# Kernel optimization log

Hardware: AMD Instinct MI355X
Metric: run time of the kernel (lower is better)

The kernel has to match this reference:

```python
import jax, jax.numpy as jnp
import numpy as np

D_MODEL = 1024
D_HEAD = 64
B, S = 4, 2048


def setup_inputs() -> dict:
    key = jax.random.key(0)
    k1, k2, k3, k4 = jax.random.split(key, 4)
    residual_stream = jax.random.normal(k1, (B, S, D_MODEL), dtype=jnp.float32)
    # torch.nn.Linear weights are [out_features, in_features]
    Wq = jax.random.normal(k2, (D_HEAD, D_MODEL), dtype=jnp.float32) * 0.02
    Wk = jax.random.normal(k3, (D_HEAD, D_MODEL), dtype=jnp.float32) * 0.02
    Wv = jax.random.normal(k4, (D_HEAD, D_MODEL), dtype=jnp.float32) * 0.02
    return {"residual_stream": residual_stream, "Wq": Wq, "Wk": Wk, "Wv": Wv}


def reference(residual_stream, Wq, Wk, Wv):
    # Linear projections (no bias): y = x @ W.T
    q = jnp.einsum('bsd,hd->bsh', residual_stream, Wq)  # [B,S,d_head]
    k = jnp.einsum('bsd,hd->bsh', residual_stream, Wk)
    v = jnp.einsum('bsd,hd->bsh', residual_stream, Wv)
    # NOTE: module scales by 1/sqrt(d_model), not 1/sqrt(d_head)
    scale = 1.0 / jnp.sqrt(jnp.float32(D_MODEL))
    scores = jnp.einsum('bqh,bkh->bqk', q, k) * scale  # [B,S,S]
    # causal mask: lower-triangular allowed
    s = residual_stream.shape[1]
    causal = jnp.tril(jnp.ones((s, s), dtype=bool))
    scores = jnp.where(causal[None, :, :], scores, -jnp.inf)
    attn = jax.nn.softmax(scores, axis=-1)
    # dropout_chance=0.0 (eval/deterministic) -> identity
    return jnp.einsum('bqk,bkh->bqh', attn, v)  # [B,S,d_head]
```

## Files before the change

### kernel.cpp

```cpp
#include <hip/hip_runtime.h>
#include <hip/hip_bf16.h>

#define NB 4
#define SEQ 2048
#define DM 1024
#define DH 64

typedef __attribute__((ext_vector_type(8))) short bf16x8;
typedef __attribute__((ext_vector_type(4))) float f32x4;
typedef __attribute__((ext_vector_type(4))) short short4v;

__device__ inline short f2bf(float f) {
  union { float f; unsigned u; } x; x.f = f;
  unsigned r = x.u + 0x7FFFu + ((x.u >> 16) & 1u);
  return (short)(r >> 16);
}

__global__ __launch_bounds__(256) void wconv_kernel(
    const float* __restrict__ Wq, const float* __restrict__ Wk,
    const float* __restrict__ Wv, short* __restrict__ wbf)
{
  const int tid = blockIdx.x * 256 + threadIdx.x;
  const int base = tid * 8;
  const int row = base >> 10;
  const int col = base & 1023;
  const float* src = (row < 64) ? Wq : (row < 128) ? Wk : Wv;
  src += (size_t)(row & 63) * DM + col;
  f32x4 f0 = ((const f32x4*)src)[0];
  f32x4 f1 = ((const f32x4*)src)[1];
  bf16x8 h = { f2bf(f0[0]), f2bf(f0[1]), f2bf(f0[2]), f2bf(f0[3]),
               f2bf(f1[0]), f2bf(f1[1]), f2bf(f1[2]), f2bf(f1[3]) };
  *(bf16x8*)(wbf + (size_t)row * DM + col) = h;
}

__global__ __launch_bounds__(512) void proj_kernel(
    const float* __restrict__ X, const short* __restrict__ wbf,
    short* __restrict__ qout, short* __restrict__ kout,
    short* __restrict__ vtout)
{
  __shared__ short x_lds[2][32][80];
  __shared__ short w_lds[2][192][80];

  const int t = threadIdx.x;
  const int l = t & 63;
  const int w = t >> 6;
  const int m0 = blockIdx.x * 32;

  f32x4 acc[3];
#pragma unroll
  for (int i = 0; i < 3; i++) acc[i] = (f32x4){0.f, 0.f, 0.f, 0.f};

  const int xr = t >> 4;
  const int xc = (t & 15) * 4;
  const int wr = t >> 3;
  const int wc = (t & 7) * 8;

  const float* xsrc  = X   + (size_t)(m0 + xr) * DM + xc;
  const short* wsrc0 = wbf + (size_t)(wr)       * DM + wc;
  const short* wsrc1 = wbf + (size_t)(64 + wr)  * DM + wc;
  const short* wsrc2 = wbf + (size_t)(128 + wr) * DM + wc;

  {
    f32x4 f = *(const f32x4*)xsrc;
    short4v h = { f2bf(f[0]), f2bf(f[1]), f2bf(f[2]), f2bf(f[3]) };
    *(short4v*)&x_lds[0][xr][xc] = h;
    *(bf16x8*)&w_lds[0][wr][wc]       = *(const bf16x8*)wsrc0;
    *(bf16x8*)&w_lds[0][64 + wr][wc]  = *(const bf16x8*)wsrc1;
    *(bf16x8*)&w_lds[0][128 + wr][wc] = *(const bf16x8*)wsrc2;
  }
  f32x4 xA = *(const f32x4*)(xsrc + 64);
  bf16x8 wA0 = *(const bf16x8*)(wsrc0 + 64);
  bf16x8 wA1 = *(const bf16x8*)(wsrc1 + 64);
  bf16x8 wA2 = *(const bf16x8*)(wsrc2 + 64);
  f32x4 xB;
  bf16x8 wB0, wB1, wB2;
  __syncthreads();

#pragma unroll
  for (int it = 0; it < 16; it++) {
    const int buf = it & 1;
    const int k2 = (it + 2) * 64;

    if ((it & 1) == 0) {
      if (it + 2 < 16) {
        xB  = *(const f32x4*)(xsrc + k2);
        wB0 = *(const bf16x8*)(wsrc0 + k2);
        wB1 = *(const bf16x8*)(wsrc1 + k2);
        wB2 = *(const bf16x8*)(wsrc2 + k2);
      }
    } else {
      if (it + 2 < 16) {
        xA  = *(const f32x4*)(xsrc + k2);
        wA0 = *(const bf16x8*)(wsrc0 + k2);
        wA1 = *(const bf16x8*)(wsrc1 + k2);
        wA2 = *(const bf16x8*)(wsrc2 + k2);
      }
    }

    const short* xp = &x_lds[buf][(w & 1) * 16 + (l & 15)][(l >> 4) << 3];
    bf16x8 a0 = *(const bf16x8*)xp;
    bf16x8 a1 = *(const bf16x8*)(xp + 32);
#pragma unroll
    for (int nf = 0; nf < 3; nf++) {
      const int cf = (w >> 1) * 3 + nf;
      const short* wp = &w_lds[buf][cf * 16 + (l & 15)][(l >> 4) << 3];
      bf16x8 b0 = *(const bf16x8*)wp;
      bf16x8 b1 = *(const bf16x8*)(wp + 32);
      acc[nf] = __builtin_amdgcn_mfma_f32_16x16x32_bf16(a0, b0, acc[nf], 0, 0, 0);
      acc[nf] = __builtin_amdgcn_mfma_f32_16x16x32_bf16(a1, b1, acc[nf], 0, 0, 0);
    }

    if (it < 15) {
      if ((it & 1) == 0) {
        short4v h = { f2bf(xA[0]), f2bf(xA[1]), f2bf(xA[2]), f2bf(xA[3]) };
        *(short4v*)&x_lds[buf ^ 1][xr][xc] = h;
        *(bf16x8*)&w_lds[buf ^ 1][wr][wc]       = wA0;
        *(bf16x8*)&w_lds[buf ^ 1][64 + wr][wc]  = wA1;
        *(bf16x8*)&w_lds[buf ^ 1][128 + wr][wc] = wA2;
      } else {
        short4v h = { f2bf(xB[0]), f2bf(xB[1]), f2bf(xB[2]), f2bf(xB[3]) };
        *(short4v*)&x_lds[buf ^ 1][xr][xc] = h;
        *(bf16x8*)&w_lds[buf ^ 1][wr][wc]       = wB0;
        *(bf16x8*)&w_lds[buf ^ 1][64 + wr][wc]  = wB1;
        *(bf16x8*)&w_lds[buf ^ 1][128 + wr][wc] = wB2;
      }
    }
    __syncthreads();
  }

  const int rowb = m0 + (w & 1) * 16 + ((l >> 4) << 2);
#pragma unroll
  for (int nf = 0; nf < 3; nf++) {
    const int c = ((w >> 1) * 3 + nf) * 16 + (l & 15);
#pragma unroll
    for (int j = 0; j < 4; j++) {
      const int row = rowb + j;
      const float v = acc[nf][j];
      if (c < 64) {
        qout[row * DH + c] = f2bf(v * 0.03125f);
      } else if (c < 128) {
        kout[row * DH + (c - 64)] = f2bf(v);
      } else {
        const int b = row >> 11, s = row & (SEQ - 1);
        vtout[b * (DH * SEQ) + (c - 128) * SEQ + s] = f2bf(v);
      }
    }
  }
}

__global__ __launch_bounds__(256) void flash_kernel(
    const short* __restrict__ qin, const short* __restrict__ kin,
    const short* __restrict__ vtin, float* __restrict__ po,
    float* __restrict__ pm, float* __restrict__ pl,
    const int nck, const int cht)
{
  __shared__ short k_lds[2][64][72];
  __shared__ short vt_lds[2][64][72];
  __shared__ short p_lds[4][16][72];

  const int qt = blockIdx.x;
  const int ck = blockIdx.y;
  const int t0 = ck * cht;
  if (t0 > qt) return;
  const int b = blockIdx.z;

  const int t = threadIdx.x;
  const int l = t & 63;
  const int w = t >> 6;
  const int q0 = qt * 64;
  const int tend = min(t0 + cht, qt + 1);

  const short* qb = qin  + (size_t)b * SEQ * DH;
  const short* kb = kin  + (size_t)b * SEQ * DH;
  const short* vb = vtin + (size_t)b * DH * SEQ;

  const short* qr = qb + (size_t)(q0 + w * 16 + (l & 15)) * DH + ((l >> 4) << 3);
  const bf16x8 qf0 = *(const bf16x8*)qr;
  const bf16x8 qf1 = *(const bf16x8*)(qr + 32);

  f32x4 o[4];
#pragma unroll
  for (int i = 0; i < 4; i++) o[i] = (f32x4){0.f, 0.f, 0.f, 0.f};
  float m_run[4] = {-1e30f, -1e30f, -1e30f, -1e30f};
  float l_run[4] = {0.f, 0.f, 0.f, 0.f};

  const int sr = t >> 3;
  const int sc = (t & 7) * 8;

  {
    const int j0 = t0 * 64;
#pragma unroll
    for (int i = 0; i < 2; i++) {
      const int r = sr + i * 32;
      *(bf16x8*)&k_lds[0][r][sc]  = *(const bf16x8*)(kb + (size_t)(j0 + r) * DH + sc);
      *(bf16x8*)&vt_lds[0][r][sc] = *(const bf16x8*)(vb + (size_t)r * SEQ + j0 + sc);
    }
  }
  __syncthreads();

  for (int tt = t0; tt < tend; tt++) {
    const int bi = (tt - t0) & 1;
    const int j0 = tt * 64;
    const bool pf = (tt + 1 < tend);

    bf16x8 kpf0, kpf1, vpf0, vpf1;
    if (pf) {
      const int j1 = j0 + 64;
      kpf0 = *(const bf16x8*)(kb + (size_t)(j1 + sr) * DH + sc);
      kpf1 = *(const bf16x8*)(kb + (size_t)(j1 + sr + 32) * DH + sc);
      vpf0 = *(const bf16x8*)(vb + (size_t)sr * SEQ + j1 + sc);
      vpf1 = *(const bf16x8*)(vb + (size_t)(sr + 32) * SEQ + j1 + sc);
    }

    f32x4 s[4];
#pragma unroll
    for (int nf = 0; nf < 4; nf++) {
      const short* kr = &k_lds[bi][nf * 16 + (l & 15)][(l >> 4) << 3];
      bf16x8 b0 = *(const bf16x8*)kr;
      bf16x8 b1 = *(const bf16x8*)(kr + 32);
      f32x4 a = (f32x4){0.f, 0.f, 0.f, 0.f};
      a = __builtin_amdgcn_mfma_f32_16x16x32_bf16(qf0, b0, a, 0, 0, 0);
      a = __builtin_amdgcn_mfma_f32_16x16x32_bf16(qf1, b1, a, 0, 0, 0);
      s[nf] = a;
    }

    {
      const int growb = q0 + w * 16 + ((l >> 4) << 2);
#pragma unroll
      for (int nf = 0; nf < 4; nf++) {
        const int gcol = j0 + nf * 16 + (l & 15);
#pragma unroll
        for (int j = 0; j < 4; j++)
          if (gcol > growb + j) s[nf][j] = -1e30f;
      }
    }

    float alpha[4];
#pragma unroll
    for (int j = 0; j < 4; j++) {
      float tm = fmaxf(fmaxf(s[0][j], s[1][j]), fmaxf(s[2][j], s[3][j]));
      tm = fmaxf(tm, __shfl_xor(tm, 1));
      tm = fmaxf(tm, __shfl_xor(tm, 2));
      tm = fmaxf(tm, __shfl_xor(tm, 4));
      tm = fmaxf(tm, __shfl_xor(tm, 8));
      const float mn = fmaxf(m_run[j], tm);
      alpha[j] = exp2f((m_run[j] - mn) * 1.44269504f);
      m_run[j] = mn;
      float rs = 0.f;
#pragma unroll
      for (int nf = 0; nf < 4; nf++) {
        const float p = exp2f((s[nf][j] - mn) * 1.44269504f);
        s[nf][j] = p;
        rs += p;
      }
      rs += __shfl_xor(rs, 1);
      rs += __shfl_xor(rs, 2);
      rs += __shfl_xor(rs, 4);
      rs += __shfl_xor(rs, 8);
      l_run[j] = l_run[j] * alpha[j] + rs;
    }
#pragma unroll
    for (int df = 0; df < 4; df++)
#pragma unroll
      for (int j = 0; j < 4; j++) o[df][j] *= alpha[j];

#pragma unroll
    for (int nf = 0; nf < 4; nf++)
#pragma unroll
      for (int j = 0; j < 4; j++)
        p_lds[w][((l >> 4) << 2) + j][nf * 16 + (l & 15)] = f2bf(s[nf][j]);

    asm volatile("s_waitcnt lgkmcnt(0)" ::: "memory");
    __builtin_amdgcn_sched_barrier(0);

#pragma unroll
    for (int ks = 0; ks < 2; ks++) {
      const short* pr = &p_lds[w][l & 15][ks * 32 + ((l >> 4) << 3)];
      const bf16x8 pa = *(const bf16x8*)pr;
#pragma unroll
      for (int df = 0; df < 4; df++) {
        const short* vr = &vt_lds[bi][df * 16 + (l & 15)][ks * 32 + ((l >> 4) << 3)];
        const bf16x8 vf = *(const bf16x8*)vr;
        o[df] = __builtin_amdgcn_mfma_f32_16x16x32_bf16(pa, vf, o[df], 0, 0, 0);
      }
    }

    if (pf) {
      *(bf16x8*)&k_lds[bi ^ 1][sr][sc]       = kpf0;
      *(bf16x8*)&k_lds[bi ^ 1][sr + 32][sc]  = kpf1;
      *(bf16x8*)&vt_lds[bi ^ 1][sr][sc]      = vpf0;
      *(bf16x8*)&vt_lds[bi ^ 1][sr + 32][sc] = vpf1;
    }
    __syncthreads();
  }

  const int rowb = q0 + w * 16 + ((l >> 4) << 2);
#pragma unroll
  for (int j = 0; j < 4; j++) {
    const size_t rowg = (size_t)b * SEQ + rowb + j;
#pragma unroll
    for (int df = 0; df < 4; df++)
      po[(rowg * nck + ck) * DH + df * 16 + (l & 15)] = o[df][j];
    if ((l & 15) == 0) {
      pm[rowg * nck + ck] = m_run[j];
      pl[rowg * nck + ck] = l_run[j];
    }
  }
}

__global__ __launch_bounds__(256) void merge_kernel(
    const float* __restrict__ po, const float* __restrict__ pm,
    const float* __restrict__ pl, float* __restrict__ out,
    const int nck, const int ckshift)
{
  const int gid = blockIdx.x * 256 + threadIdx.x;
  const int r = gid >> 6;
  const int d = gid & 63;
  const int s = r & (SEQ - 1);
  const int C = (s >> ckshift) + 1;

  float m = -1e30f;
  for (int c = 0; c < C; c++) m = fmaxf(m, pm[r * nck + c]);
  float den = 0.f, num = 0.f;
  for (int c = 0; c < C; c++) {
    const float wgt = exp2f((pm[r * nck + c] - m) * 1.44269504f);
    den += pl[r * nck + c] * wgt;
    num += po[(size_t)(r * nck + c) * DH + d] * wgt;
  }
  out[gid] = num / den;
}

extern "C" void kernel_launch(void* const* d_in, const int* in_sizes, int n_in,
                              void* d_out, int out_size, void* d_ws, size_t ws_size,
                              hipStream_t stream) {
  const float* X  = (const float*)d_in[0];
  const float* Wq = (const float*)d_in[1];
  const float* Wk = (const float*)d_in[2];
  const float* Wv = (const float*)d_in[3];

  const size_t nrow = (size_t)NB * SEQ;
  short* qws  = (short*)d_ws;
  short* kws  = qws + nrow * DH;
  short* vtws = kws + nrow * DH;
  float* po   = (float*)(vtws + nrow * DH);
  short* wbf  = (short*)po;
  const size_t qkv_bytes = 3 * nrow * DH * sizeof(short);

  int nck, cht, ckshift;
  {
    const size_t need4 = qkv_bytes + nrow * 4 * (DH + 2) * sizeof(float);
    if (ws_size >= need4) { nck = 4; cht = 8;  ckshift = 9;  }
    else                  { nck = 1; cht = 32; ckshift = 11; }
  }
  float* pm = po + nrow * nck * DH;
  float* pl = pm + nrow * nck;

  wconv_kernel<<<dim3(96), 256, 0, stream>>>(Wq, Wk, Wv, wbf);
  proj_kernel<<<dim3(NB * SEQ / 32), 512, 0, stream>>>(X, wbf, qws, kws, vtws);
  flash_kernel<<<dim3(SEQ / 64, nck, NB), 256, 0, stream>>>(qws, kws, vtws, po, pm, pl, nck, cht);
  merge_kernel<<<dim3(NB * SEQ * DH / 256), 256, 0, stream>>>(po, pm, pl, (float*)d_out, nck, ckshift);
}
```

Baseline: 48.48 us.

## Split projection GEMM over K into two slices with separate reduce kernel

New measurement: 53.96 us. +11.3%, slower.

```diff
diff --git a/kernel.cpp b/kernel.cpp
--- a/kernel.cpp
+++ b/kernel.cpp
@@ -14,6 +14,12 @@
   union { float f; unsigned u; } x; x.f = f;
   unsigned r = x.u + 0x7FFFu + ((x.u >> 16) & 1u);
   return (short)(r >> 16);
+}
+
+__device__ inline float bf2f(short s) {
+  union { unsigned u; float f; } x;
+  x.u = ((unsigned)(unsigned short)s) << 16;
+  return x.f;
 }
 
 __global__ __launch_bounds__(256) void wconv_kernel(
@@ -35,16 +41,17 @@
 
 __global__ __launch_bounds__(512) void proj_kernel(
     const float* __restrict__ X, const short* __restrict__ wbf,
-    short* __restrict__ qout, short* __restrict__ kout,
-    short* __restrict__ vtout)
-{
-  __shared__ short x_lds[2][32][80];
-  __shared__ short w_lds[2][192][80];
+    short* __restrict__ pacc)
+{
+  __shared__ short x_lds[2][32][72];
+  __shared__ short w_lds[2][192][72];
 
   const int t = threadIdx.x;
   const int l = t & 63;
   const int w = t >> 6;
   const int m0 = blockIdx.x * 32;
+  const int ks = blockIdx.y;
+  const int kbase = ks * 512;
 
   f32x4 acc[3];
 #pragma unroll
@@ -55,10 +62,10 @@
   const int wr = t >> 3;
   const int wc = (t & 7) * 8;
 
-  const float* xsrc  = X   + (size_t)(m0 + xr) * DM + xc;
-  const short* wsrc0 = wbf + (size_t)(wr)       * DM + wc;
-  const short* wsrc1 = wbf + (size_t)(64 + wr)  * DM + wc;
-  const short* wsrc2 = wbf + (size_t)(128 + wr) * DM + wc;
+  const float* xsrc  = X   + (size_t)(m0 + xr) * DM + kbase + xc;
+  const short* wsrc0 = wbf + (size_t)(wr)       * DM + kbase + wc;
+  const short* wsrc1 = wbf + (size_t)(64 + wr)  * DM + kbase + wc;
+  const short* wsrc2 = wbf + (size_t)(128 + wr) * DM + kbase + wc;
 
   {
     f32x4 f = *(const f32x4*)xsrc;
@@ -77,19 +84,19 @@
   __syncthreads();
 
 #pragma unroll
-  for (int it = 0; it < 16; it++) {
+  for (int it = 0; it < 8; it++) {
     const int buf = it & 1;
     const int k2 = (it + 2) * 64;
 
     if ((it & 1) == 0) {
-      if (it + 2 < 16) {
+      if (it + 2 < 8) {
         xB  = *(const f32x4*)(xsrc + k2);
         wB0 = *(const bf16x8*)(wsrc0 + k2);
         wB1 = *(const bf16x8*)(wsrc1 + k2);
         wB2 = *(const bf16x8*)(wsrc2 + k2);
       }
     } else {
-      if (it + 2 < 16) {
+      if (it + 2 < 8) {
         xA  = *(const f32x4*)(xsrc + k2);
         wA0 = *(const bf16x8*)(wsrc0 + k2);
         wA1 = *(const bf16x8*)(wsrc1 + k2);
@@ -110,7 +117,7 @@
       acc[nf] = __builtin_amdgcn_mfma_f32_16x16x32_bf16(a1, b1, acc[nf], 0, 0, 0);
     }
 
-    if (it < 15) {
+    if (it < 7) {
       if ((it & 1) == 0) {
         short4v h = { f2bf(xA[0]), f2bf(xA[1]), f2bf(xA[2]), f2bf(xA[3]) };
         *(short4v*)&x_lds[buf ^ 1][xr][xc] = h;
@@ -128,23 +135,47 @@
     __syncthreads();
   }
 
+  short* pp = pacc + (size_t)ks * (NB * SEQ) * 192;
   const int rowb = m0 + (w & 1) * 16 + ((l >> 4) << 2);
 #pragma unroll
   for (int nf = 0; nf < 3; nf++) {
     const int c = ((w >> 1) * 3 + nf) * 16 + (l & 15);
 #pragma unroll
-    for (int j = 0; j < 4; j++) {
-      const int row = rowb + j;
-      const float v = acc[nf][j];
-      if (c < 64) {
-        qout[row * DH + c] = f2bf(v * 0.03125f);
-      } else if (c < 128) {
-        kout[row * DH + (c - 64)] = f2bf(v);
-      } else {
-        const int b = row >> 11, s = row & (SEQ - 1);
-        vtout[b * (DH * SEQ) + (c - 128) * SEQ + s] = f2bf(v);
-      }
-    }
+    for (int j = 0; j < 4; j++)
+      pp[(size_t)(rowb + j) * 192 + c] = f2bf(acc[nf][j]);
+  }
+}
+
+__global__ __launch_bounds__(256) void reduce_kernel(
+    const short* __restrict__ pacc, short* __restrict__ qout,
+    short* __restrict__ kout, short* __restrict__ vtout)
+{
+  const int gid = blockIdx.x * 256 + threadIdx.x;
+  const int r = gid / 48;
+  const int cg = gid - r * 48;
+  const int c0 = cg * 4;
+
+  const short4v a = *(const short4v*)(pacc + (size_t)r * 192 + c0);
+  const short4v b = *(const short4v*)(pacc + ((size_t)(NB * SEQ) + r) * 192 + c0);
+  float v0 = bf2f(a[0]) + bf2f(b[0]);
+  float v1 = bf2f(a[1]) + bf2f(b[1]);
+  float v2 = bf2f(a[2]) + bf2f(b[2]);
+  float v3 = bf2f(a[3]) + bf2f(b[3]);
+
+  if (c0 < 64) {
+    short4v h = { f2bf(v0 * 0.03125f), f2bf(v1 * 0.03125f),
+                  f2bf(v2 * 0.03125f), f2bf(v3 * 0.03125f) };
+    *(short4v*)(qout + (size_t)r * DH + c0) = h;
+  } else if (c0 < 128) {
+    short4v h = { f2bf(v0), f2bf(v1), f2bf(v2), f2bf(v3) };
+    *(short4v*)(kout + (size_t)r * DH + (c0 - 64)) = h;
+  } else {
+    const int bb = r >> 11, s = r & (SEQ - 1);
+    short* vt = vtout + (size_t)bb * DH * SEQ + (size_t)(c0 - 128) * SEQ + s;
+    vt[0 * SEQ] = f2bf(v0);
+    vt[1 * SEQ] = f2bf(v1);
+    vt[2 * SEQ] = f2bf(v2);
+    vt[3 * SEQ] = f2bf(v3);
   }
 }
 
@@ -342,8 +373,9 @@
   short* qws  = (short*)d_ws;
   short* kws  = qws + nrow * DH;
   short* vtws = kws + nrow * DH;
-  float* po   = (float*)(vtws + nrow * DH);
-  short* wbf  = (short*)po;
+  short* pacc = vtws + nrow * DH;
+  short* wbf  = pacc + 2 * nrow * 192;
+  float* po   = (float*)pacc;
   const size_t qkv_bytes = 3 * nrow * DH * sizeof(short);
 
   int nck, cht, ckshift;
@@ -356,7 +388,8 @@
   float* pl = pm + nrow * nck;
 
   wconv_kernel<<<dim3(96), 256, 0, stream>>>(Wq, Wk, Wv, wbf);
-  proj_kernel<<<dim3(NB * SEQ / 32), 512, 0, stream>>>(X, wbf, qws, kws, vtws);
+  proj_kernel<<<dim3(NB * SEQ / 32, 2), 512, 0, stream>>>(X, wbf, pacc);
+  reduce_kernel<<<dim3(nrow * 48 / 256), 256, 0, stream>>>(pacc, qws, kws, vtws);
   flash_kernel<<<dim3(SEQ / 64, nck, NB), 256, 0, stream>>>(qws, kws, vtws, po, pm, pl, nck, cht);
   merge_kernel<<<dim3(NB * SEQ * DH / 256), 256, 0, stream>>>(po, pm, pl, (float*)d_out, nck, ckshift);
 }
```

## Split projection GEMM along K with resident weight tiles and separate reduce kernel

Applied to the files above, without the earlier changes.

After: 55.72 us. +14.9%, slower.

```diff
diff --git a/kernel.cpp b/kernel.cpp
--- a/kernel.cpp
+++ b/kernel.cpp
@@ -14,6 +14,12 @@
   union { float f; unsigned u; } x; x.f = f;
   unsigned r = x.u + 0x7FFFu + ((x.u >> 16) & 1u);
   return (short)(r >> 16);
+}
+
+__device__ inline float bf2f(short s) {
+  union { unsigned u; float f; } x;
+  x.u = ((unsigned)(unsigned short)s) << 16;
+  return x.f;
 }
 
 __global__ __launch_bounds__(256) void wconv_kernel(
@@ -33,7 +39,145 @@
   *(bf16x8*)(wbf + (size_t)row * DM + col) = h;
 }
 
-__global__ __launch_bounds__(512) void proj_kernel(
+__global__ __launch_bounds__(512) void proj_v3_kernel(
+    const float* __restrict__ X, const short* __restrict__ wbf,
+    short* __restrict__ pacc)
+{
+  __shared__ short w_lds[192][264];
+  __shared__ short x_lds[2][32][264];
+
+  const int t = threadIdx.x;
+  const int l = t & 63;
+  const int w = t >> 6;
+  const int ks = blockIdx.y;
+  const int kbase = ks * 256;
+  const int mbase = blockIdx.x * 128;
+
+#pragma unroll
+  for (int i = 0; i < 12; i++) {
+    const int idx = t + i * 512;
+    const int row = idx >> 5;
+    const int cb = idx & 31;
+    *(bf16x8*)&w_lds[row][cb * 8] =
+        *(const bf16x8*)(wbf + (size_t)row * DM + kbase + cb * 8);
+  }
+
+  const int xr0 = t >> 6;
+  const int xc0 = (t & 63) * 4;
+
+  f32x4 xp0, xp1, xp2, xp3;
+  {
+    const float* base = X + (size_t)(mbase + xr0) * DM + kbase + xc0;
+    xp0 = *(const f32x4*)(base + 0 * 8 * DM);
+    xp1 = *(const f32x4*)(base + 1 * 8 * DM);
+    xp2 = *(const f32x4*)(base + 2 * 8 * DM);
+    xp3 = *(const f32x4*)(base + 3 * 8 * DM);
+  }
+  {
+    short4v h0 = { f2bf(xp0[0]), f2bf(xp0[1]), f2bf(xp0[2]), f2bf(xp0[3]) };
+    short4v h1 = { f2bf(xp1[0]), f2bf(xp1[1]), f2bf(xp1[2]), f2bf(xp1[3]) };
+    short4v h2 = { f2bf(xp2[0]), f2bf(xp2[1]), f2bf(xp2[2]), f2bf(xp2[3]) };
+    short4v h3 = { f2bf(xp3[0]), f2bf(xp3[1]), f2bf(xp3[2]), f2bf(xp3[3]) };
+    *(short4v*)&x_lds[0][xr0 + 0][xc0]  = h0;
+    *(short4v*)&x_lds[0][xr0 + 8][xc0]  = h1;
+    *(short4v*)&x_lds[0][xr0 + 16][xc0] = h2;
+    *(short4v*)&x_lds[0][xr0 + 24][xc0] = h3;
+  }
+  __syncthreads();
+
+  const int arow = (w & 1) * 16 + (l & 15);
+  const int kk = (l >> 4) << 3;
+  const int cg = (w >> 1) * 3;
+  short* pp = pacc + (size_t)ks * (NB * SEQ) * 192;
+
+#pragma unroll
+  for (int mt = 0; mt < 4; mt++) {
+    const int buf = mt & 1;
+
+    if (mt < 3) {
+      const float* base = X + (size_t)(mbase + (mt + 1) * 32 + xr0) * DM + kbase + xc0;
+      xp0 = *(const f32x4*)(base + 0 * 8 * DM);
+      xp1 = *(const f32x4*)(base + 1 * 8 * DM);
+      xp2 = *(const f32x4*)(base + 2 * 8 * DM);
+      xp3 = *(const f32x4*)(base + 3 * 8 * DM);
+    }
+
+    f32x4 acc0 = (f32x4){0.f, 0.f, 0.f, 0.f};
+    f32x4 acc1 = (f32x4){0.f, 0.f, 0.f, 0.f};
+    f32x4 acc2 = (f32x4){0.f, 0.f, 0.f, 0.f};
+#pragma unroll
+    for (int k8 = 0; k8 < 8; k8++) {
+      const int kc = k8 * 32 + kk;
+      bf16x8 a  = *(const bf16x8*)&x_lds[buf][arow][kc];
+      bf16x8 b0 = *(const bf16x8*)&w_lds[(cg + 0) * 16 + (l & 15)][kc];
+      acc0 = __builtin_amdgcn_mfma_f32_16x16x32_bf16(a, b0, acc0, 0, 0, 0);
+      bf16x8 b1 = *(const bf16x8*)&w_lds[(cg + 1) * 16 + (l & 15)][kc];
+      acc1 = __builtin_amdgcn_mfma_f32_16x16x32_bf16(a, b1, acc1, 0, 0, 0);
+      bf16x8 b2 = *(const bf16x8*)&w_lds[(cg + 2) * 16 + (l & 15)][kc];
+      acc2 = __builtin_amdgcn_mfma_f32_16x16x32_bf16(a, b2, acc2, 0, 0, 0);
+    }
+
+    {
+      const int rowb = mbase + mt * 32 + (w & 1) * 16 + ((l >> 4) << 2);
+      const int c0 = (cg + 0) * 16 + (l & 15);
+      const int c1 = (cg + 1) * 16 + (l & 15);
+      const int c2 = (cg + 2) * 16 + (l & 15);
+#pragma unroll
+      for (int j = 0; j < 4; j++) {
+        pp[(size_t)(rowb + j) * 192 + c0] = f2bf(acc0[j]);
+        pp[(size_t)(rowb + j) * 192 + c1] = f2bf(acc1[j]);
+        pp[(size_t)(rowb + j) * 192 + c2] = f2bf(acc2[j]);
+      }
+    }
+
+    if (mt < 3) {
+      short4v h0 = { f2bf(xp0[0]), f2bf(xp0[1]), f2bf(xp0[2]), f2bf(xp0[3]) };
+      short4v h1 = { f2bf(xp1[0]), f2bf(xp1[1]), f2bf(xp1[2]), f2bf(xp1[3]) };
+      short4v h2 = { f2bf(xp2[0]), f2bf(xp2[1]), f2bf(xp2[2]), f2bf(xp2[3]) };
+      short4v h3 = { f2bf(xp3[0]), f2bf(xp3[1]), f2bf(xp3[2]), f2bf(xp3[3]) };
+      *(short4v*)&x_lds[buf ^ 1][xr0 + 0][xc0]  = h0;
+      *(short4v*)&x_lds[buf ^ 1][xr0 + 8][xc0]  = h1;
+      *(short4v*)&x_lds[buf ^ 1][xr0 + 16][xc0] = h2;
+      *(short4v*)&x_lds[buf ^ 1][xr0 + 24][xc0] = h3;
+    }
+    __syncthreads();
+  }
+}
+
+__global__ __launch_bounds__(256) void reduce4_kernel(
+    const short* __restrict__ pacc, short* __restrict__ qout,
+    short* __restrict__ kout, short* __restrict__ vtout)
+{
+  const int gid = blockIdx.x * 256 + threadIdx.x;
+  const int r = gid / 48;
+  const int cg = gid - r * 48;
+  const int c0 = cg * 4;
+
+  float v0 = 0.f, v1 = 0.f, v2 = 0.f, v3 = 0.f;
+#pragma unroll
+  for (int s = 0; s < 4; s++) {
+    const short4v a = *(const short4v*)(pacc + ((size_t)s * (NB * SEQ) + r) * 192 + c0);
+    v0 += bf2f(a[0]); v1 += bf2f(a[1]); v2 += bf2f(a[2]); v3 += bf2f(a[3]);
+  }
+
+  if (c0 < 64) {
+    short4v h = { f2bf(v0 * 0.03125f), f2bf(v1 * 0.03125f),
+                  f2bf(v2 * 0.03125f), f2bf(v3 * 0.03125f) };
+    *(short4v*)(qout + (size_t)r * DH + c0) = h;
+  } else if (c0 < 128) {
+    short4v h = { f2bf(v0), f2bf(v1), f2bf(v2), f2bf(v3) };
+    *(short4v*)(kout + (size_t)r * DH + (c0 - 64)) = h;
+  } else {
+    const int bb = r >> 11, s = r & (SEQ - 1);
+    short* vt = vtout + (size_t)bb * DH * SEQ + (size_t)(c0 - 128) * SEQ + s;
+    vt[0 * SEQ] = f2bf(v0);
+    vt[1 * SEQ] = f2bf(v1);
+    vt[2 * SEQ] = f2bf(v2);
+    vt[3 * SEQ] = f2bf(v3);
+  }
+}
+
+__global__ __launch_bounds__(512) void proj_fb_kernel(
     const float* __restrict__ X, const short* __restrict__ wbf,
     short* __restrict__ qout, short* __restrict__ kout,
     short* __restrict__ vtout)
@@ -342,21 +486,37 @@
   short* qws  = (short*)d_ws;
   short* kws  = qws + nrow * DH;
   short* vtws = kws + nrow * DH;
-  float* po   = (float*)(vtws + nrow * DH);
-  short* wbf  = (short*)po;
   const size_t qkv_bytes = 3 * nrow * DH * sizeof(short);
 
-  int nck, cht, ckshift;
-  {
+  const size_t big_need = qkv_bytes + 4 * nrow * 192 * sizeof(short)
+                        + 192 * DM * sizeof(short);
+
+  if (ws_size >= big_need) {
+    short* pacc = vtws + nrow * DH;
+    short* wbf  = pacc + 4 * nrow * 192;
+    float* po   = (float*)pacc;
+    float* pm   = po + nrow * 4 * DH;
+    float* pl   = pm + nrow * 4;
+
+    wconv_kernel<<<dim3(96), 256, 0, stream>>>(Wq, Wk, Wv, wbf);
+    proj_v3_kernel<<<dim3(64, 4), 512, 0, stream>>>(X, wbf, pacc);
+    reduce4_kernel<<<dim3((int)(nrow * 48 / 256)), 256, 0, stream>>>(pacc, qws, kws, vtws);
+    flash_kernel<<<dim3(SEQ / 64, 4, NB), 256, 0, stream>>>(qws, kws, vtws, po, pm, pl, 4, 8);
+    merge_kernel<<<dim3(NB * SEQ * DH / 256), 256, 0, stream>>>(po, pm, pl, (float*)d_out, 4, 9);
+  } else {
+    float* po  = (float*)(vtws + nrow * DH);
+    short* wbf = (short*)po;
+
+    int nck, cht, ckshift;
     const size_t need4 = qkv_bytes + nrow * 4 * (DH + 2) * sizeof(float);
     if (ws_size >= need4) { nck = 4; cht = 8;  ckshift = 9;  }
     else                  { nck = 1; cht = 32; ckshift = 11; }
-  }
-  float* pm = po + nrow * nck * DH;
-  float* pl = pm + nrow * nck;
-
-  wconv_kernel<<<dim3(96), 256, 0, stream>>>(Wq, Wk, Wv, wbf);
-  proj_kernel<<<dim3(NB * SEQ / 32), 512, 0, stream>>>(X, wbf, qws, kws, vtws);
-  flash_kernel<<<dim3(SEQ / 64, nck, NB), 256, 0, stream>>>(qws, kws, vtws, po, pm, pl, nck, cht);
-  merge_kernel<<<dim3(NB * SEQ * DH / 256), 256, 0, stream>>>(po, pm, pl, (float*)d_out, nck, ckshift);
-}
+    float* pm = po + nrow * nck * DH;
+    float* pl = pm + nrow * nck;
+
+    wconv_kernel<<<dim3(96), 256, 0, stream>>>(Wq, Wk, Wv, wbf);
+    proj_fb_kernel<<<dim3(NB * SEQ / 32), 512, 0, stream>>>(X, wbf, qws, kws, vtws);
+    flash_kernel<<<dim3(SEQ / 64, nck, NB), 256, 0, stream>>>(qws, kws, vtws, po, pm, pl, nck, cht);
+    merge_kernel<<<dim3(NB * SEQ * DH / 256), 256, 0, stream>>>(po, pm, pl, (float*)d_out, nck, ckshift);
+  }
+}
```

## Fuse split-K merge into flash kernel via last-block atomic counter

Applied to the files above, without the earlier changes.

After: 182.7 us. +276.9%, slower.

```diff
diff --git a/kernel.cpp b/kernel.cpp
--- a/kernel.cpp
+++ b/kernel.cpp
@@ -18,8 +18,12 @@
 
 __global__ __launch_bounds__(256) void wconv_kernel(
     const float* __restrict__ Wq, const float* __restrict__ Wk,
-    const float* __restrict__ Wv, short* __restrict__ wbf)
+    const float* __restrict__ Wv, short* __restrict__ wbf,
+    int* __restrict__ cnt)
 {
+  if (blockIdx.x == 0 && threadIdx.x < NB * 32)
+    cnt[threadIdx.x] = 0;
+
   const int tid = blockIdx.x * 256 + threadIdx.x;
   const int base = tid * 8;
   const int row = base >> 10;
@@ -152,11 +156,13 @@
     const short* __restrict__ qin, const short* __restrict__ kin,
     const short* __restrict__ vtin, float* __restrict__ po,
     float* __restrict__ pm, float* __restrict__ pl,
+    int* __restrict__ cnt, float* __restrict__ out,
     const int nck, const int cht)
 {
   __shared__ short k_lds[2][64][72];
   __shared__ short vt_lds[2][64][72];
   __shared__ short p_lds[4][16][72];
+  __shared__ int winner_sh;
 
   const int qt = blockIdx.x;
   const int ck = blockIdx.y;
@@ -306,28 +312,31 @@
       pl[rowg * nck + ck] = l_run[j];
     }
   }
-}
-
-__global__ __launch_bounds__(256) void merge_kernel(
-    const float* __restrict__ po, const float* __restrict__ pm,
-    const float* __restrict__ pl, float* __restrict__ out,
-    const int nck, const int ckshift)
-{
-  const int gid = blockIdx.x * 256 + threadIdx.x;
-  const int r = gid >> 6;
-  const int d = gid & 63;
-  const int s = r & (SEQ - 1);
-  const int C = (s >> ckshift) + 1;
-
-  float m = -1e30f;
-  for (int c = 0; c < C; c++) m = fmaxf(m, pm[r * nck + c]);
-  float den = 0.f, num = 0.f;
-  for (int c = 0; c < C; c++) {
-    const float wgt = exp2f((pm[r * nck + c] - m) * 1.44269504f);
-    den += pl[r * nck + c] * wgt;
-    num += po[(size_t)(r * nck + c) * DH + d] * wgt;
-  }
-  out[gid] = num / den;
+
+  __threadfence();
+  const int C = qt / cht + 1;
+  if (t == 0) {
+    const int old = atomicAdd(&cnt[b * 32 + qt], 1);
+    winner_sh = (old == C - 1);
+  }
+  __syncthreads();
+  if (!winner_sh) return;
+  __threadfence();
+
+  for (int i = t; i < 64 * DH; i += 256) {
+    const int r = q0 + (i >> 6);
+    const int d = i & 63;
+    const size_t rowg = (size_t)b * SEQ + r;
+    float m = -1e30f;
+    for (int c = 0; c < C; c++) m = fmaxf(m, pm[rowg * nck + c]);
+    float den = 0.f, num = 0.f;
+    for (int c = 0; c < C; c++) {
+      const float wgt = exp2f((pm[rowg * nck + c] - m) * 1.44269504f);
+      den += pl[rowg * nck + c] * wgt;
+      num += po[(rowg * nck + c) * DH + d] * wgt;
+    }
+    out[rowg * DH + d] = num / den;
+  }
 }
 
 extern "C" void kernel_launch(void* const* d_in, const int* in_sizes, int n_in,
@@ -342,21 +351,24 @@
   short* qws  = (short*)d_ws;
   short* kws  = qws + nrow * DH;
   short* vtws = kws + nrow * DH;
-  float* po   = (float*)(vtws + nrow * DH);
-  short* wbf  = (short*)po;
   const size_t qkv_bytes = 3 * nrow * DH * sizeof(short);
 
-  int nck, cht, ckshift;
+  int nck, cht;
   {
-    const size_t need4 = qkv_bytes + nrow * 4 * (DH + 2) * sizeof(float);
-    if (ws_size >= need4) { nck = 4; cht = 8;  ckshift = 9;  }
-    else                  { nck = 1; cht = 32; ckshift = 11; }
-  }
-  float* pm = po + nrow * nck * DH;
-  float* pl = pm + nrow * nck;
-
-  wconv_kernel<<<dim3(96), 256, 0, stream>>>(Wq, Wk, Wv, wbf);
+    const size_t need8 = qkv_bytes + nrow * 8 * (DH + 2) * sizeof(float) + 512;
+    const size_t need4 = qkv_bytes + nrow * 4 * (DH + 2) * sizeof(float) + 512;
+    if      (ws_size >= need8) { nck = 8; cht = 4;  }
+    else if (ws_size >= need4) { nck = 4; cht = 8;  }
+    else                       { nck = 1; cht = 32; }
+  }
+  float* po  = (float*)(vtws + nrow * DH);
+  short* wbf = (short*)po;
+  float* pm  = po + nrow * nck * DH;
+  float* pl  = pm + nrow * nck;
+  int*   cnt = (int*)(pl + nrow * nck);
+
+  wconv_kernel<<<dim3(96), 256, 0, stream>>>(Wq, Wk, Wv, wbf, cnt);
   proj_kernel<<<dim3(NB * SEQ / 32), 512, 0, stream>>>(X, wbf, qws, kws, vtws);
-  flash_kernel<<<dim3(SEQ / 64, nck, NB), 256, 0, stream>>>(qws, kws, vtws, po, pm, pl, nck, cht);
-  merge_kernel<<<dim3(NB * SEQ * DH / 256), 256, 0, stream>>>(po, pm, pl, (float*)d_out, nck, ckshift);
-}
+  flash_kernel<<<dim3(SEQ / 64, nck, NB), 256, 0, stream>>>(
+      qws, kws, vtws, po, pm, pl, cnt, (float*)d_out, nck, cht);
+}
```
